# Optimization experiments

Hardware: AMD Instinct MI355X
Metric: run time of the kernel (lower is better)

Reference implementation:

```python
import jax, jax.numpy as jnp
import numpy as np

T, D, E, H = 16384, 1024, 8, 4096  # tokens, embed, experts, ffn hidden
CAP_FACTOR = 1


def setup_inputs() -> dict:
    key = jax.random.key(0)
    ks = jax.random.split(key, 10)
    s = lambda k, shp, fan: jax.random.normal(k, shp, jnp.float32) * (1.0 / np.sqrt(fan))
    return {
        "x": jax.random.normal(ks[0], (T, D), jnp.float32),
        # Router: Linear(D,D) -> relu -> Linear(D,E) -> softmax
        "wr1": s(ks[1], (D, D), D),
        "br1": jnp.zeros((D,), jnp.float32),
        "wr2": s(ks[2], (D, E), D),
        "br2": jnp.zeros((E,), jnp.float32),
        # Per-expert FFN: Linear(D,H) -> relu -> Linear(H,D)
        "w1": s(ks[3], (E, D, H), D),
        "b1": jnp.zeros((E, H), jnp.float32),
        "w2": s(ks[4], (E, H, D), H),
        "b2": jnp.zeros((E, D), jnp.float32),
    }


def reference(x, wr1, br1, wr2, br2, w1, b1, w2, b2):
    Tn, Dn = x.shape
    En = w1.shape[0]
    C = (CAP_FACTOR * Tn) // En  # expert capacity

    # Router probabilities [T, E]
    probs = jax.nn.softmax(jnp.maximum(x @ wr1 + br1, 0.0) @ wr2 + br2, axis=1)
    eid = jnp.argmax(probs, axis=-1)  # top-1 expert per token

    # Position of each token within its expert's queue (deterministic
    # first-come capacity dropping in place of torch randperm selection).
    onehot = jax.nn.one_hot(eid, En, dtype=jnp.int32)  # [T, E]
    pos = jnp.sum(jnp.cumsum(onehot, axis=0) * onehot, axis=1) - 1  # [T]
    valid = pos < C

    # Build dispatch index table idx[e, c] = token id (sentinel T = empty slot)
    slot = jnp.where(valid, eid * C + pos, En * C)  # out-of-range => dropped
    flat = jnp.full((En * C,), Tn, dtype=jnp.int32)
    flat = flat.at[slot].set(jnp.arange(Tn, dtype=jnp.int32), mode="drop")
    idx = flat.reshape(En, C)

    # Gather tokens (padded zero row for empty slots) -> [E, C, D]
    xp = jnp.concatenate([x, jnp.zeros((1, Dn), x.dtype)], axis=0)
    xe = xp[idx]

    # Grouped-expert FFN
    h = jnp.maximum(jnp.einsum("ecd,edh->ech", xe, w1) + b1[:, None, :], 0.0)
    oe = jnp.einsum("ech,ehd->ecd", h, w2) + b2[:, None, :]

    # Gating scores for kept tokens; zero for empty slots
    probs_p = jnp.concatenate([probs, jnp.zeros((1, En), probs.dtype)], axis=0)
    gate = probs_p[idx, jnp.arange(En, dtype=jnp.int32)[:, None]]  # [E, C]
    gate = jnp.where(idx < Tn, gate, 0.0)
    oe = oe * gate[:, :, None]

    # Scatter-combine back to token order; dropped tokens stay zero
    out = jnp.zeros_like(x).at[idx.reshape(-1)].add(
        oe.reshape(En * C, Dn), mode="drop")
    return out
```

## Files before the change

### kernel.cpp

```cpp
#include <hip/hip_runtime.h>

typedef short s16x8 __attribute__((ext_vector_type(8)));
typedef float f32x4 __attribute__((ext_vector_type(4)));
typedef unsigned short u16;
typedef u16 u16x8 __attribute__((ext_vector_type(8)));

constexpr int TN = 16384;
constexpr int DN = 1024;
constexpr int EN = 8;
constexpr int HN = 4096;
constexpr int CAPN = 2048;

#define GLOAD16(g, l) __builtin_amdgcn_global_load_lds( \
    (const __attribute__((address_space(1))) unsigned int*)(g), \
    (__attribute__((address_space(3))) unsigned int*)(l), 16, 0, 0)

__device__ __forceinline__ u16 f2bf(float x){
  unsigned u = __float_as_uint(x);
  u = (u + 0x7fffu + ((u >> 16) & 1u)) >> 16;
  return (u16)u;
}

__global__ __launch_bounds__(256) void k_transpose(const float* __restrict__ in, u16* __restrict__ out,
                                                   int R, int C){
  __shared__ float tile[64][65];
  const int e = blockIdx.z;
  const int r0 = blockIdx.y * 64, c0 = blockIdx.x * 64;
  const float* ine = in + (size_t)e * R * C;
  u16* oute = out + (size_t)e * R * C;
  const int t = threadIdx.x;
  {
    const int dr = t >> 2, cs = (t & 3) * 16;
    const float* src = ine + (size_t)(r0 + dr) * C + (c0 + cs);
    #pragma unroll
    for (int i = 0; i < 4; ++i){
      f32x4 v = *reinterpret_cast<const f32x4*>(src + i * 4);
      #pragma unroll
      for (int c = 0; c < 4; ++c) tile[dr][cs + i*4 + c] = v[c];
    }
  }
  __syncthreads();
  {
    const int dn = t >> 2, ks = (t & 3) * 16;
    u16x8 lo, hi;
    #pragma unroll
    for (int i = 0; i < 8; ++i) lo[i] = f2bf(tile[ks + i][dn]);
    #pragma unroll
    for (int i = 0; i < 8; ++i) hi[i] = f2bf(tile[ks + 8 + i][dn]);
    u16* dst = oute + (size_t)(c0 + dn) * R + (r0 + ks);
    *reinterpret_cast<u16x8*>(dst) = lo;
    *reinterpret_cast<u16x8*>(dst + 8) = hi;
  }
}

__global__ __launch_bounds__(256) void k_router_gemm1(const float* __restrict__ X, const float* __restrict__ W,
                                                      const float* __restrict__ bias, float* __restrict__ Y){
  __shared__ float As[32][128];
  __shared__ float Bs[32][128];
  const int m0 = blockIdx.y * 128, n0 = blockIdx.x * 128;
  const int t = threadIdx.x;
  const int tx = t & 15, ty = t >> 4;
  float acc[8][8] = {};
  const int am = t >> 1, aseg = (t & 1) * 16;
  for (int k0 = 0; k0 < DN; k0 += 32){
    f32x4 av[4], bv[4];
    #pragma unroll
    for (int i = 0; i < 4; ++i)
      av[i] = *reinterpret_cast<const f32x4*>(X + (size_t)(m0 + am) * DN + k0 + aseg + i*4);
    #pragma unroll
    for (int j = 0; j < 4; ++j){
      int flat = t + 256*j;
      int kb = flat >> 5, nb = (flat & 31) * 4;
      bv[j] = *reinterpret_cast<const f32x4*>(W + (size_t)(k0 + kb) * DN + n0 + nb);
    }
    __syncthreads();
    #pragma unroll
    for (int i = 0; i < 4; ++i)
      #pragma unroll
      for (int c = 0; c < 4; ++c)
        As[aseg + i*4 + c][am] = av[i][c];
    #pragma unroll
    for (int j = 0; j < 4; ++j){
      int flat = t + 256*j;
      int kb = flat >> 5, nb = (flat & 31) * 4;
      *reinterpret_cast<f32x4*>(&Bs[kb][nb]) = bv[j];
    }
    __syncthreads();
    #pragma unroll
    for (int k = 0; k < 32; ++k){
      float a[8], b[8];
      *reinterpret_cast<f32x4*>(a)     = *reinterpret_cast<const f32x4*>(&As[k][ty*4]);
      *reinterpret_cast<f32x4*>(a + 4) = *reinterpret_cast<const f32x4*>(&As[k][64 + ty*4]);
      *reinterpret_cast<f32x4*>(b)     = *reinterpret_cast<const f32x4*>(&Bs[k][tx*4]);
      *reinterpret_cast<f32x4*>(b + 4) = *reinterpret_cast<const f32x4*>(&Bs[k][64 + tx*4]);
      #pragma unroll
      for (int i = 0; i < 8; ++i)
        #pragma unroll
        for (int jj = 0; jj < 8; ++jj)
          acc[i][jj] = fmaf(a[i], b[jj], acc[i][jj]);
    }
  }
  float bcol[8];
  #pragma unroll
  for (int j = 0; j < 4; ++j){ bcol[j] = bias[n0 + tx*4 + j]; bcol[4+j] = bias[n0 + 64 + tx*4 + j]; }
  #pragma unroll
  for (int i = 0; i < 8; ++i){
    const int row = m0 + (i < 4 ? ty*4 + i : 64 + ty*4 + (i - 4));
    float* dst = Y + (size_t)row * DN + n0;
    f32x4 v0, v1;
    #pragma unroll
    for (int j = 0; j < 4; ++j){ float v = acc[i][j] + bcol[j];     v0[j] = v > 0.f ? v : 0.f; }
    #pragma unroll
    for (int j = 0; j < 4; ++j){ float v = acc[i][4+j] + bcol[4+j]; v1[j] = v > 0.f ? v : 0.f; }
    *reinterpret_cast<f32x4*>(dst + tx*4)      = v0;
    *reinterpret_cast<f32x4*>(dst + 64 + tx*4) = v1;
  }
}

__global__ __launch_bounds__(256) void k_router_logits(const float* __restrict__ R1, const float* __restrict__ W2,
                                                       const float* __restrict__ B2, int* __restrict__ eid,
                                                       float* __restrict__ gate){
  __shared__ float w2s[EN][DN];
  __shared__ float b2s[EN];
  const int t = threadIdx.x;
  #pragma unroll
  for (int j = 0; j < 32; ++j){
    int flat = t + 256*j;
    w2s[flat & 7][flat >> 3] = W2[flat];
  }
  if (t < EN) b2s[t] = B2[t];
  __syncthreads();
  const int wid = t >> 6, lane = t & 63;
  const int token = blockIdx.x * 4 + wid;
  const float* row = R1 + (size_t)token * DN;
  float acc[8] = {};
  for (int i = 0; i < 16; ++i){
    int k = lane + 64*i;
    float v = row[k];
    #pragma unroll
    for (int e = 0; e < 8; ++e) acc[e] = fmaf(v, w2s[e][k], acc[e]);
  }
  #pragma unroll
  for (int e = 0; e < 8; ++e){
    float s = acc[e];
    #pragma unroll
    for (int off = 32; off > 0; off >>= 1) s += __shfl_xor(s, off);
    acc[e] = s + b2s[e];
  }
  float best = acc[0]; int be = 0;
  #pragma unroll
  for (int e = 1; e < 8; ++e) if (acc[e] > best){ best = acc[e]; be = e; }
  float sum = 0.f;
  #pragma unroll
  for (int e = 0; e < 8; ++e) sum += __expf(acc[e] - best);
  if (lane == 0){ eid[token] = be; gate[token] = 1.0f / sum; }
}

__global__ __launch_bounds__(256) void k_count(const int* __restrict__ eid, int* __restrict__ counts){
  __shared__ int h[EN];
  const int t = threadIdx.x;
  if (t < EN) h[t] = 0;
  __syncthreads();
  atomicAdd(&h[eid[blockIdx.x * 256 + t]], 1);
  __syncthreads();
  if (t < EN) counts[blockIdx.x * EN + t] = h[t];
}

__global__ void k_scan(const int* __restrict__ counts, int* __restrict__ offs){
  const int e = threadIdx.x;
  if (e < EN){
    int run = 0;
    for (int c = 0; c < TN/256; ++c){
      offs[c * EN + e] = run;
      run += counts[c * EN + e];
    }
  }
}

__global__ __launch_bounds__(256) void k_assign(const int* __restrict__ eid, const int* __restrict__ offs,
                                                int* __restrict__ idx){
  __shared__ int wcnt[4][EN];
  const int t = threadIdx.x;
  const int w = t >> 6, lane = t & 63;
  const int token = blockIdx.x * 256 + t;
  const int e = eid[token];
  unsigned long long mymask = 0;
  #pragma unroll
  for (int ee = 0; ee < EN; ++ee){
    unsigned long long m = __ballot(e == ee);
    if (ee == e) mymask = m;
    if (lane == 0) wcnt[w][ee] = __popcll(m);
  }
  const int rank = __popcll(mymask & ((1ull << lane) - 1ull));
  __syncthreads();
  int pre = 0;
  for (int wi = 0; wi < w; ++wi) pre += wcnt[wi][e];
  const int pos = offs[blockIdx.x * EN + e] + pre + rank;
  if (pos < CAPN) idx[e * CAPN + pos] = token;
}

__global__ __launch_bounds__(256) void k_gather(const float* __restrict__ X, const int* __restrict__ idx,
                                                u16* __restrict__ xe){
  const int slot = blockIdx.x;
  const int tok = idx[slot];
  const int t = threadIdx.x;
  unsigned lo = 0, hi = 0;
  if (tok >= 0){
    f32x4 v = *reinterpret_cast<const f32x4*>(X + (size_t)tok * DN + t*4);
    lo = (unsigned)f2bf(v[0]) | ((unsigned)f2bf(v[1]) << 16);
    hi = (unsigned)f2bf(v[2]) | ((unsigned)f2bf(v[3]) << 16);
  }
  uint2 o; o.x = lo; o.y = hi;
  *reinterpret_cast<uint2*>(xe + (size_t)slot * DN + t*4) = o;
}

template<int EPI>
__global__ __launch_bounds__(256) void k_ffn(const u16* __restrict__ A, const u16* __restrict__ Bt,
                                             const float* __restrict__ bias, const int* __restrict__ idx,
                                             const float* __restrict__ gate, u16* __restrict__ Hout,
                                             float* __restrict__ Out, int K, int N){
  __shared__ u16 As[128 * 32];
  __shared__ u16 Bs[128 * 32];
  const int e = blockIdx.z;
  const int m0 = blockIdx.y * 128, n0 = blockIdx.x * 128;
  const u16* Ae = A + ((size_t)e * CAPN + m0) * K;
  const u16* Be = Bt + ((size_t)e * N + n0) * K;
  const int t = threadIdx.x;
  const int wid = t >> 6, lane = t & 63;
  const int wr = wid >> 1, wc = wid & 1;
  const int r16 = lane & 15, kseg = lane >> 4;
  f32x4 acc[4][4] = {};
  const u16* ga = Ae + (size_t)(t >> 2) * K + (t & 3) * 8;
  const u16* gb = Be + (size_t)(t >> 2) * K + (t & 3) * 8;
  char* AsB = (char*)As + wid * 1024;
  char* BsB = (char*)Bs + wid * 1024;
  for (int k0 = 0; k0 < K; k0 += 32){
    __syncthreads();
    GLOAD16(ga + k0,                AsB);
    GLOAD16(ga + (size_t)64*K + k0, AsB + 4096);
    GLOAD16(gb + k0,                BsB);
    GLOAD16(gb + (size_t)64*K + k0, BsB + 4096);
    __syncthreads();
    s16x8 af[4], bf[4];
    #pragma unroll
    for (int fr = 0; fr < 4; ++fr)
      af[fr] = *reinterpret_cast<const s16x8*>(&As[(wr*64 + fr*16 + r16) * 32 + kseg*8]);
    #pragma unroll
    for (int fc = 0; fc < 4; ++fc)
      bf[fc] = *reinterpret_cast<const s16x8*>(&Bs[(wc*64 + fc*16 + r16) * 32 + kseg*8]);
    #pragma unroll
    for (int fr = 0; fr < 4; ++fr)
      #pragma unroll
      for (int fc = 0; fc < 4; ++fc)
        acc[fr][fc] = __builtin_amdgcn_mfma_f32_16x16x32_bf16(af[fr], bf[fc], acc[fr][fc], 0, 0, 0);
  }
  if (EPI == 0){
    #pragma unroll
    for (int fc = 0; fc < 4; ++fc){
      const int col = n0 + wc*64 + fc*16 + r16;
      const float bc = bias[e * N + col];
      #pragma unroll
      for (int fr = 0; fr < 4; ++fr){
        #pragma unroll
        for (int r = 0; r < 4; ++r){
          const int row = m0 + wr*64 + fr*16 + kseg*4 + r;
          float v = acc[fr][fc][r] + bc;
          v = v > 0.f ? v : 0.f;
          Hout[((size_t)e * CAPN + row) * N + col] = f2bf(v);
        }
      }
    }
  } else {
    #pragma unroll
    for (int fr = 0; fr < 4; ++fr){
      #pragma unroll
      for (int r = 0; r < 4; ++r){
        const int row = m0 + wr*64 + fr*16 + kseg*4 + r;
        const int tok = idx[e * CAPN + row];
        if (tok < 0) continue;
        const float g = gate[tok];
        #pragma unroll
        for (int fc = 0; fc < 4; ++fc){
          const int col = n0 + wc*64 + fc*16 + r16;
          Out[(size_t)tok * DN + col] = (acc[fr][fc][r] + bias[e * N + col]) * g;
        }
      }
    }
  }
}

extern "C" void kernel_launch(void* const* d_in, const int* in_sizes, int n_in,
                              void* d_out, int out_size, void* d_ws, size_t ws_size,
                              hipStream_t stream){
  const float* x   = (const float*)d_in[0];
  const float* wr1 = (const float*)d_in[1];
  const float* br1 = (const float*)d_in[2];
  const float* wr2 = (const float*)d_in[3];
  const float* br2 = (const float*)d_in[4];
  const float* w1  = (const float*)d_in[5];
  const float* b1  = (const float*)d_in[6];
  const float* w2  = (const float*)d_in[7];
  const float* b2  = (const float*)d_in[8];
  float* out = (float*)d_out;

  char* ws = (char*)d_ws;
  size_t off = 0;
  auto walloc = [&](size_t bytes) -> void* {
    void* p = ws + off;
    off += (bytes + 255) & ~(size_t)255;
    return p;
  };
  u16* hbuf   = (u16*)walloc((size_t)EN * CAPN * HN * 2);
  float* r1   = (float*)hbuf;
  u16* xe     = (u16*)walloc((size_t)EN * CAPN * DN * 2);
  u16* w1T    = (u16*)walloc((size_t)EN * HN * DN * 2);
  u16* w2T    = (u16*)walloc((size_t)EN * HN * DN * 2);
  int* eid    = (int*)walloc(TN * 4);
  float* gate = (float*)walloc(TN * 4);
  int* counts = (int*)walloc((TN/256) * EN * 4);
  int* offs   = (int*)walloc((TN/256) * EN * 4);
  int* idx    = (int*)walloc(EN * CAPN * 4);
  (void)in_sizes; (void)n_in; (void)out_size; (void)ws_size;

  k_transpose<<<dim3(HN/64, DN/64, EN), 256, 0, stream>>>(w1, w1T, DN, HN);
  k_transpose<<<dim3(DN/64, HN/64, EN), 256, 0, stream>>>(w2, w2T, HN, DN);
  k_router_gemm1<<<dim3(DN/128, TN/128), 256, 0, stream>>>(x, wr1, br1, r1);
  k_router_logits<<<dim3(TN/4), 256, 0, stream>>>(r1, wr2, br2, eid, gate);
  k_count<<<dim3(TN/256), 256, 0, stream>>>(eid, counts);
  k_scan<<<dim3(1), 64, 0, stream>>>(counts, offs);
  hipMemsetAsync(idx, 0xFF, (size_t)EN * CAPN * 4, stream);
  k_assign<<<dim3(TN/256), 256, 0, stream>>>(eid, offs, idx);
  k_gather<<<dim3(EN * CAPN), 256, 0, stream>>>(x, idx, xe);
  k_ffn<0><<<dim3(HN/128, CAPN/128, EN), 256, 0, stream>>>(xe, w1T, b1, nullptr, nullptr, hbuf, nullptr, DN, HN);
  hipMemsetAsync(d_out, 0, (size_t)TN * DN * 4, stream);
  k_ffn<1><<<dim3(DN/128, CAPN/128, EN), 256, 0, stream>>>(hbuf, w2T, b2, idx, gate, nullptr, out, HN, DN);
}
```

Baseline: 1.217 ms.

## Run router GEMM on bf16 MFMA with 3-way split and fuse gather into FFN1

Replaces the fp32 FMA router GEMM with a bf16 MFMA kernel that splits each operand into three bf16 parts and sums six cross products, aiming for near-fp32 accuracy at matrix-core throughput. The split of x is also reused as the bf16 source for the expert FFN, and the separate gather kernel is removed: FFN1 loads token rows directly through idx, with a zero row for empty slots. This removes the slow scalar router GEMM and one gather pass, at the cost of extra split kernels, triple operand traffic in the router, and reduced accuracy versus true fp32 if the split is insufficient.

```diff
diff --git a/kernel.cpp b/kernel.cpp
--- a/kernel.cpp
+++ b/kernel.cpp
@@ -4,6 +4,7 @@
 typedef float f32x4 __attribute__((ext_vector_type(4)));
 typedef unsigned short u16;
 typedef u16 u16x8 __attribute__((ext_vector_type(8)));
+typedef u16 u16x4 __attribute__((ext_vector_type(4)));
 
 constexpr int TN = 16384;
 constexpr int DN = 1024;
@@ -19,6 +20,13 @@
   unsigned u = __float_as_uint(x);
   u = (u + 0x7fffu + ((u >> 16) & 1u)) >> 16;
   return (u16)u;
+}
+
+__device__ __forceinline__ void split3(float x, u16& h, u16& l, u16& l2){
+  h = f2bf(x);
+  float r = x - __uint_as_float((unsigned)h << 16);
+  l = f2bf(r);
+  l2 = f2bf(r - __uint_as_float((unsigned)l << 16));
 }
 
 __global__ __launch_bounds__(256) void k_transpose(const float* __restrict__ in, u16* __restrict__ out,
@@ -53,67 +61,119 @@
   }
 }
 
-__global__ __launch_bounds__(256) void k_router_gemm1(const float* __restrict__ X, const float* __restrict__ W,
-                                                      const float* __restrict__ bias, float* __restrict__ Y){
-  __shared__ float As[32][128];
-  __shared__ float Bs[32][128];
+__global__ __launch_bounds__(256) void k_split_x(const float* __restrict__ X, u16* __restrict__ H,
+                                                 u16* __restrict__ L, u16* __restrict__ L2){
+  const size_t i = ((size_t)blockIdx.x * 256 + threadIdx.x) * 4;
+  f32x4 v = *reinterpret_cast<const f32x4*>(X + i);
+  u16x4 h, l, l2;
+  #pragma unroll
+  for (int j = 0; j < 4; ++j){ u16 a, b, c; split3(v[j], a, b, c); h[j] = a; l[j] = b; l2[j] = c; }
+  *reinterpret_cast<u16x4*>(H + i)  = h;
+  *reinterpret_cast<u16x4*>(L + i)  = l;
+  *reinterpret_cast<u16x4*>(L2 + i) = l2;
+}
+
+__global__ __launch_bounds__(256) void k_split_wT(const float* __restrict__ in, u16* __restrict__ oh,
+                                                  u16* __restrict__ ol, u16* __restrict__ ol2){
+  __shared__ float tile[64][65];
+  const int r0 = blockIdx.y * 64, c0 = blockIdx.x * 64;
+  const int t = threadIdx.x;
+  {
+    const int dr = t >> 2, cs = (t & 3) * 16;
+    const float* src = in + (size_t)(r0 + dr) * DN + (c0 + cs);
+    #pragma unroll
+    for (int i = 0; i < 4; ++i){
+      f32x4 v = *reinterpret_cast<const f32x4*>(src + i * 4);
+      #pragma unroll
+      for (int c = 0; c < 4; ++c) tile[dr][cs + i*4 + c] = v[c];
+    }
+  }
+  __syncthreads();
+  {
+    const int dn = t >> 2, ks = (t & 3) * 16;
+    u16x8 h0, h1, l0, l1, m0v, m1v;
+    #pragma unroll
+    for (int i = 0; i < 8; ++i){ u16 a,b,c; split3(tile[ks + i][dn], a,b,c);     h0[i]=a; l0[i]=b; m0v[i]=c; }
+    #pragma unroll
+    for (int i = 0; i < 8; ++i){ u16 a,b,c; split3(tile[ks + 8 + i][dn], a,b,c); h1[i]=a; l1[i]=b; m1v[i]=c; }
+    const size_t o = (size_t)(c0 + dn) * DN + (r0 + ks);
+    *reinterpret_cast<u16x8*>(oh + o) = h0;  *reinterpret_cast<u16x8*>(oh + o + 8) = h1;
+    *reinterpret_cast<u16x8*>(ol + o) = l0;  *reinterpret_cast<u16x8*>(ol + o + 8) = l1;
+    *reinterpret_cast<u16x8*>(ol2 + o) = m0v; *reinterpret_cast<u16x8*>(ol2 + o + 8) = m1v;
+  }
+}
+
+__global__ __launch_bounds__(256) void k_router_mfma(
+    const u16* __restrict__ Ah, const u16* __restrict__ Al, const u16* __restrict__ Al2,
+    const u16* __restrict__ Bh, const u16* __restrict__ Bl, const u16* __restrict__ Bl2,
+    const float* __restrict__ bias, float* __restrict__ Y){
+  constexpr int K = DN;
+  __shared__ u16 As[3 * 128 * 32];
+  __shared__ u16 Bs[3 * 128 * 32];
   const int m0 = blockIdx.y * 128, n0 = blockIdx.x * 128;
   const int t = threadIdx.x;
-  const int tx = t & 15, ty = t >> 4;
-  float acc[8][8] = {};
-  const int am = t >> 1, aseg = (t & 1) * 16;
-  for (int k0 = 0; k0 < DN; k0 += 32){
-    f32x4 av[4], bv[4];
-    #pragma unroll
-    for (int i = 0; i < 4; ++i)
-      av[i] = *reinterpret_cast<const f32x4*>(X + (size_t)(m0 + am) * DN + k0 + aseg + i*4);
-    #pragma unroll
-    for (int j = 0; j < 4; ++j){
-      int flat = t + 256*j;
-      int kb = flat >> 5, nb = (flat & 31) * 4;
-      bv[j] = *reinterpret_cast<const f32x4*>(W + (size_t)(k0 + kb) * DN + n0 + nb);
-    }
+  const int wid = t >> 6, lane = t & 63;
+  const int wr = wid >> 1, wc = wid & 1;
+  const int r16 = lane & 15, kseg = lane >> 4;
+  f32x4 acc[4][4] = {};
+  const size_t aoff = (size_t)(m0 + (t >> 2)) * K + (t & 3) * 8;
+  const size_t boff = (size_t)(n0 + (t >> 2)) * K + (t & 3) * 8;
+  const u16* gah = Ah + aoff;  const u16* gal = Al + aoff;  const u16* gam = Al2 + aoff;
+  const u16* gbh = Bh + boff;  const u16* gbl = Bl + boff;  const u16* gbm = Bl2 + boff;
+  char* A0 = (char*)As + wid * 1024;  char* A1 = A0 + 8192;  char* A2 = A1 + 8192;
+  char* B0 = (char*)Bs + wid * 1024;  char* B1 = B0 + 8192;  char* B2 = B1 + 8192;
+  constexpr size_t R64 = (size_t)64 * K;
+  for (int k0 = 0; k0 < K; k0 += 32){
     __syncthreads();
-    #pragma unroll
-    for (int i = 0; i < 4; ++i)
-      #pragma unroll
-      for (int c = 0; c < 4; ++c)
-        As[aseg + i*4 + c][am] = av[i][c];
-    #pragma unroll
-    for (int j = 0; j < 4; ++j){
-      int flat = t + 256*j;
-      int kb = flat >> 5, nb = (flat & 31) * 4;
-      *reinterpret_cast<f32x4*>(&Bs[kb][nb]) = bv[j];
-    }
+    GLOAD16(gah + k0, A0); GLOAD16(gah + R64 + k0, A0 + 4096);
+    GLOAD16(gal + k0, A1); GLOAD16(gal + R64 + k0, A1 + 4096);
+    GLOAD16(gam + k0, A2); GLOAD16(gam + R64 + k0, A2 + 4096);
+    GLOAD16(gbh + k0, B0); GLOAD16(gbh + R64 + k0, B0 + 4096);
+    GLOAD16(gbl + k0, B1); GLOAD16(gbl + R64 + k0, B1 + 4096);
+    GLOAD16(gbm + k0, B2); GLOAD16(gbm + R64 + k0, B2 + 4096);
     __syncthreads();
-    #pragma unroll
-    for (int k = 0; k < 32; ++k){
-      float a[8], b[8];
-      *reinterpret_cast<f32x4*>(a)     = *reinterpret_cast<const f32x4*>(&As[k][ty*4]);
-      *reinterpret_cast<f32x4*>(a + 4) = *reinterpret_cast<const f32x4*>(&As[k][64 + ty*4]);
-      *reinterpret_cast<f32x4*>(b)     = *reinterpret_cast<const f32x4*>(&Bs[k][tx*4]);
-      *reinterpret_cast<f32x4*>(b + 4) = *reinterpret_cast<const f32x4*>(&Bs[k][64 + tx*4]);
-      #pragma unroll
-      for (int i = 0; i < 8; ++i)
-        #pragma unroll
-        for (int jj = 0; jj < 8; ++jj)
-          acc[i][jj] = fmaf(a[i], b[jj], acc[i][jj]);
-    }
-  }
-  float bcol[8];
-  #pragma unroll
-  for (int j = 0; j < 4; ++j){ bcol[j] = bias[n0 + tx*4 + j]; bcol[4+j] = bias[n0 + 64 + tx*4 + j]; }
-  #pragma unroll
-  for (int i = 0; i < 8; ++i){
-    const int row = m0 + (i < 4 ? ty*4 + i : 64 + ty*4 + (i - 4));
-    float* dst = Y + (size_t)row * DN + n0;
-    f32x4 v0, v1;
-    #pragma unroll
-    for (int j = 0; j < 4; ++j){ float v = acc[i][j] + bcol[j];     v0[j] = v > 0.f ? v : 0.f; }
-    #pragma unroll
-    for (int j = 0; j < 4; ++j){ float v = acc[i][4+j] + bcol[4+j]; v1[j] = v > 0.f ? v : 0.f; }
-    *reinterpret_cast<f32x4*>(dst + tx*4)      = v0;
-    *reinterpret_cast<f32x4*>(dst + 64 + tx*4) = v1;
+    s16x8 ah[4], al[4], am[4], bh[4], bl[4], bm[4];
+    #pragma unroll
+    for (int fr = 0; fr < 4; ++fr){
+      const int ro = (wr*64 + fr*16 + r16) * 32 + kseg*8;
+      ah[fr] = *reinterpret_cast<const s16x8*>(&As[ro]);
+      al[fr] = *reinterpret_cast<const s16x8*>(&As[128*32 + ro]);
+      am[fr] = *reinterpret_cast<const s16x8*>(&As[2*128*32 + ro]);
+    }
+    #pragma unroll
+    for (int fc = 0; fc < 4; ++fc){
+      const int ro = (wc*64 + fc*16 + r16) * 32 + kseg*8;
+      bh[fc] = *reinterpret_cast<const s16x8*>(&Bs[ro]);
+      bl[fc] = *reinterpret_cast<const s16x8*>(&Bs[128*32 + ro]);
+      bm[fc] = *reinterpret_cast<const s16x8*>(&Bs[2*128*32 + ro]);
+    }
+    #pragma unroll
+    for (int fr = 0; fr < 4; ++fr)
+      #pragma unroll
+      for (int fc = 0; fc < 4; ++fc){
+        f32x4 c = acc[fr][fc];
+        c = __builtin_amdgcn_mfma_f32_16x16x32_bf16(ah[fr], bh[fc], c, 0, 0, 0);
+        c = __builtin_amdgcn_mfma_f32_16x16x32_bf16(ah[fr], bl[fc], c, 0, 0, 0);
+        c = __builtin_amdgcn_mfma_f32_16x16x32_bf16(al[fr], bh[fc], c, 0, 0, 0);
+        c = __builtin_amdgcn_mfma_f32_16x16x32_bf16(al[fr], bl[fc], c, 0, 0, 0);
+        c = __builtin_amdgcn_mfma_f32_16x16x32_bf16(ah[fr], bm[fc], c, 0, 0, 0);
+        c = __builtin_amdgcn_mfma_f32_16x16x32_bf16(am[fr], bh[fc], c, 0, 0, 0);
+        acc[fr][fc] = c;
+      }
+  }
+  #pragma unroll
+  for (int fc = 0; fc < 4; ++fc){
+    const int col = n0 + wc*64 + fc*16 + r16;
+    const float bc = bias[col];
+    #pragma unroll
+    for (int fr = 0; fr < 4; ++fr){
+      #pragma unroll
+      for (int r = 0; r < 4; ++r){
+        const int row = m0 + wr*64 + fr*16 + kseg*4 + r;
+        float v = acc[fr][fc][r] + bc;
+        Y[(size_t)row * DN + col] = v > 0.f ? v : 0.f;
+      }
+    }
   }
 }
 
@@ -199,45 +259,39 @@
   if (pos < CAPN) idx[e * CAPN + pos] = token;
 }
 
-__global__ __launch_bounds__(256) void k_gather(const float* __restrict__ X, const int* __restrict__ idx,
-                                                u16* __restrict__ xe){
-  const int slot = blockIdx.x;
-  const int tok = idx[slot];
-  const int t = threadIdx.x;
-  unsigned lo = 0, hi = 0;
-  if (tok >= 0){
-    f32x4 v = *reinterpret_cast<const f32x4*>(X + (size_t)tok * DN + t*4);
-    lo = (unsigned)f2bf(v[0]) | ((unsigned)f2bf(v[1]) << 16);
-    hi = (unsigned)f2bf(v[2]) | ((unsigned)f2bf(v[3]) << 16);
-  }
-  uint2 o; o.x = lo; o.y = hi;
-  *reinterpret_cast<uint2*>(xe + (size_t)slot * DN + t*4) = o;
-}
-
 template<int EPI>
 __global__ __launch_bounds__(256) void k_ffn(const u16* __restrict__ A, const u16* __restrict__ Bt,
                                              const float* __restrict__ bias, const int* __restrict__ idx,
-                                             const float* __restrict__ gate, u16* __restrict__ Hout,
-                                             float* __restrict__ Out, int K, int N){
+                                             const float* __restrict__ gate, const u16* __restrict__ zrow,
+                                             u16* __restrict__ Hout, float* __restrict__ Out, int K, int N){
   __shared__ u16 As[128 * 32];
   __shared__ u16 Bs[128 * 32];
   const int e = blockIdx.z;
   const int m0 = blockIdx.y * 128, n0 = blockIdx.x * 128;
-  const u16* Ae = A + ((size_t)e * CAPN + m0) * K;
   const u16* Be = Bt + ((size_t)e * N + n0) * K;
   const int t = threadIdx.x;
   const int wid = t >> 6, lane = t & 63;
   const int wr = wid >> 1, wc = wid & 1;
   const int r16 = lane & 15, kseg = lane >> 4;
   f32x4 acc[4][4] = {};
-  const u16* ga = Ae + (size_t)(t >> 2) * K + (t & 3) * 8;
+  const u16 *ga0, *ga1;
+  if (EPI == 0){
+    const int s0 = e * CAPN + m0 + (t >> 2);
+    const int tok0 = idx[s0], tok1 = idx[s0 + 64];
+    ga0 = (tok0 < 0 ? zrow : A + (size_t)tok0 * K) + (t & 3) * 8;
+    ga1 = (tok1 < 0 ? zrow : A + (size_t)tok1 * K) + (t & 3) * 8;
+  } else {
+    const u16* Ae = A + ((size_t)e * CAPN + m0) * K;
+    ga0 = Ae + (size_t)(t >> 2) * K + (t & 3) * 8;
+    ga1 = ga0 + (size_t)64 * K;
+  }
   const u16* gb = Be + (size_t)(t >> 2) * K + (t & 3) * 8;
   char* AsB = (char*)As + wid * 1024;
   char* BsB = (char*)Bs + wid * 1024;
   for (int k0 = 0; k0 < K; k0 += 32){
     __syncthreads();
-    GLOAD16(ga + k0,                AsB);
-    GLOAD16(ga + (size_t)64*K + k0, AsB + 4096);
+    GLOAD16(ga0 + k0, AsB);
+    GLOAD16(ga1 + k0, AsB + 4096);
     GLOAD16(gb + k0,                BsB);
     GLOAD16(gb + (size_t)64*K + k0, BsB + 4096);
     __syncthreads();
@@ -312,26 +366,34 @@
   };
   u16* hbuf   = (u16*)walloc((size_t)EN * CAPN * HN * 2);
   float* r1   = (float*)hbuf;
-  u16* xe     = (u16*)walloc((size_t)EN * CAPN * DN * 2);
+  u16* xlo    = (u16*)((char*)hbuf + ((size_t)64 << 20));
+  u16* xlo2   = (u16*)((char*)hbuf + ((size_t)96 << 20));
+  u16* xhi    = (u16*)walloc((size_t)TN * DN * 2);
   u16* w1T    = (u16*)walloc((size_t)EN * HN * DN * 2);
   u16* w2T    = (u16*)walloc((size_t)EN * HN * DN * 2);
+  u16* wTh    = (u16*)walloc((size_t)DN * DN * 2);
+  u16* wTl    = (u16*)walloc((size_t)DN * DN * 2);
+  u16* wTl2   = (u16*)walloc((size_t)DN * DN * 2);
   int* eid    = (int*)walloc(TN * 4);
   float* gate = (float*)walloc(TN * 4);
   int* counts = (int*)walloc((TN/256) * EN * 4);
   int* offs   = (int*)walloc((TN/256) * EN * 4);
   int* idx    = (int*)walloc(EN * CAPN * 4);
+  u16* zrow   = (u16*)walloc(DN * 2);
   (void)in_sizes; (void)n_in; (void)out_size; (void)ws_size;
 
   k_transpose<<<dim3(HN/64, DN/64, EN), 256, 0, stream>>>(w1, w1T, DN, HN);
   k_transpose<<<dim3(DN/64, HN/64, EN), 256, 0, stream>>>(w2, w2T, HN, DN);
-  k_router_gemm1<<<dim3(DN/128, TN/128), 256, 0, stream>>>(x, wr1, br1, r1);
+  k_split_x<<<dim3((TN*DN)/1024), 256, 0, stream>>>(x, xhi, xlo, xlo2);
+  k_split_wT<<<dim3(DN/64, DN/64), 256, 0, stream>>>(wr1, wTh, wTl, wTl2);
+  k_router_mfma<<<dim3(DN/128, TN/128), 256, 0, stream>>>(xhi, xlo, xlo2, wTh, wTl, wTl2, br1, r1);
   k_router_logits<<<dim3(TN/4), 256, 0, stream>>>(r1, wr2, br2, eid, gate);
   k_count<<<dim3(TN/256), 256, 0, stream>>>(eid, counts);
   k_scan<<<dim3(1), 64, 0, stream>>>(counts, offs);
   hipMemsetAsync(idx, 0xFF, (size_t)EN * CAPN * 4, stream);
   k_assign<<<dim3(TN/256), 256, 0, stream>>>(eid, offs, idx);
-  k_gather<<<dim3(EN * CAPN), 256, 0, stream>>>(x, idx, xe);
-  k_ffn<0><<<dim3(HN/128, CAPN/128, EN), 256, 0, stream>>>(xe, w1T, b1, nullptr, nullptr, hbuf, nullptr, DN, HN);
+  hipMemsetAsync(zrow, 0, DN * 2, stream);
+  k_ffn<0><<<dim3(HN/128, CAPN/128, EN), 256, 0, stream>>>(xhi, w1T, b1, idx, nullptr, zrow, hbuf, nullptr, DN, HN);
   hipMemsetAsync(d_out, 0, (size_t)TN * DN * 4, stream);
-  k_ffn<1><<<dim3(DN/128, CAPN/128, EN), 256, 0, stream>>>(hbuf, w2T, b2, idx, gate, nullptr, out, HN, DN);
-}
+  k_ffn<1><<<dim3(DN/128, CAPN/128, EN), 256, 0, stream>>>(hbuf, w2T, b2, idx, gate, nullptr, nullptr, out, HN, DN);
+}
```

After: 1.048 ms. 13.9% less time.
